# Performance work log

Hardware: AMD Instinct MI355X
Metric: run time of the kernel (lower is better)

Reference implementation:

```python
import jax, jax.numpy as jnp
import numpy as np

H = 512        # hidden_size
E = 512        # embedding_size
VOCAB = 32
OPS = 16
B = 64         # batch of trees
N = 1023       # complete binary tree, depth 9 (2^10 - 1 nodes)
TEMP = 3.0
INT_TYPES_MAX = 1  # types 0 (INT_PO) and 1 (INT_NE) carry a numeric arg


def setup_inputs() -> dict:
    key = jax.random.key(0)
    ks = jax.random.split(key, 12)
    s = 0.05
    return {
        "node_types": jax.random.randint(ks[0], (B, N), 0, VOCAB),
        "node_args": jax.random.normal(ks[1], (B, N), jnp.float32),
        "validity_mask": jax.random.uniform(ks[2], (B, OPS), jnp.float32, 1e-3, 1.0),
        "emb_table": jax.random.normal(ks[3], (VOCAB, E), jnp.float32) * s,
        "W_ih": jax.random.normal(ks[4], (8 * H, E), jnp.float32) * s,
        "W_hh": jax.random.normal(ks[5], (8 * H, 2 * H), jnp.float32) * s,
        "b_ih": jax.random.normal(ks[6], (8 * H,), jnp.float32) * s,
        "b_hh": jax.random.normal(ks[7], (8 * H,), jnp.float32) * s,
        "W1": jax.random.normal(ks[8], (H, H), jnp.float32) * s,
        "b1": jax.random.normal(ks[9], (H,), jnp.float32) * s,
        "W2": jax.random.normal(ks[10], (OPS, H), jnp.float32) * s,
        "b2": jax.random.normal(ks[11], (OPS,), jnp.float32) * s,
    }


def reference(node_types, node_args, validity_mask, emb_table,
              W_ih, W_hh, b_ih, b_hh, W1, b1, W2, b2):
    # --- SympleEmbedding: per-node embedding; int-typed nodes carry arg in last slot
    emb = emb_table[node_types]                                   # [B, N, E]
    is_int = node_types <= INT_TYPES_MAX                          # [B, N]
    emb = emb.at[..., -1].set(jnp.where(is_int, node_args, emb[..., -1]))

    # --- BinaryTreeLSTM, batched level-by-level (heap layout: children of i are 2i+1, 2i+2)
    D = int(np.log2(N + 1)) - 1                                   # depth of internal levels-1 = 9
    h = jnp.zeros((B, N, H), emb.dtype)                           # leaves: zeros
    c = jnp.zeros((B, N, H), emb.dtype)
    bias = b_ih + b_hh
    for d in range(D - 1, -1, -1):                                # bottom-up over internal levels
        idx = np.arange(2 ** d - 1, 2 ** (d + 1) - 1)             # nodes at level d
        left, right = 2 * idx + 1, 2 * idx + 2
        h0 = jnp.concatenate([h[:, left], h[:, right]], axis=-1)  # [B, n, 2H]
        c0 = jnp.concatenate([c[:, left], c[:, right]], axis=-1)
        gates = (jnp.einsum('bne,ge->bng', emb[:, idx], W_ih)
                 + jnp.einsum('bnh,gh->bng', h0, W_hh) + bias)    # [B, n, 8H]
        i_g, f_g, g_g, o_g = jnp.split(gates, 4, axis=-1)         # torch LSTM gate order i,f,g,o
        c_new = jax.nn.sigmoid(f_g) * c0 + jax.nn.sigmoid(i_g) * jnp.tanh(g_g)
        h_new = jax.nn.sigmoid(o_g) * jnp.tanh(c_new)
        h = h.at[:, idx].set(h_new[..., :H])                      # keep first H (as in module)
        c = c.at[:, idx].set(c_new[..., :H])

    # --- actor FFN on root hidden + validity-masked tempered softmax
    root_h = h[:, 0]                                              # [B, H]
    x = jax.nn.relu(root_h @ W1.T + b1)
    logits = x @ W2.T + b2 + jnp.log(validity_mask)
    return jax.nn.softmax(logits / TEMP, axis=-1)                 # [B, OPS]
```

## Files before the change

kernel.cpp:

```cpp
#include <hip/hip_runtime.h>
#include <math.h>

#define Nn 1023

typedef __attribute__((ext_vector_type(8))) short short8;
typedef __attribute__((ext_vector_type(4))) float f32x4;

#define AS1(p) ((const __attribute__((address_space(1))) void*)(p))
#define AS3(p) ((__attribute__((address_space(3))) void*)(p))

__device__ __forceinline__ float sigf(float x) { return 1.0f / (1.0f + __expf(-x)); }
__device__ __forceinline__ float tanhfast(float x) {
    float e = __expf(2.0f * x);
    return 1.0f - 2.0f / (e + 1.0f);
}
__device__ __forceinline__ unsigned short f2bf(float x) {
    unsigned u = __float_as_uint(x);
    return (unsigned short)((u + 0x7fffu + ((u >> 16) & 1u)) >> 16);
}
__device__ __forceinline__ float bf2f(unsigned short b) {
    return __uint_as_float(((unsigned)b) << 16);
}

__global__ __launch_bounds__(256) void pack_whT(const float* __restrict__ W_hh,
                                                unsigned short* __restrict__ WhT) {
    int idx = blockIdx.x * 256 + threadIdx.x;
    int P = idx >> 7;
    int k0 = (idx & 127) * 8;
    int row = ((P >> 4) & 3) * 1024 + (P >> 6) * 16 + (P & 15);
    const float* src = W_hh + (size_t)row * 1024 + k0;
    float4 v0 = *(const float4*)src;
    float4 v1 = *(const float4*)(src + 4);
    short8 o;
    o[0] = (short)f2bf(v0.x); o[1] = (short)f2bf(v0.y);
    o[2] = (short)f2bf(v0.z); o[3] = (short)f2bf(v0.w);
    o[4] = (short)f2bf(v1.x); o[5] = (short)f2bf(v1.y);
    o[6] = (short)f2bf(v1.z); o[7] = (short)f2bf(v1.w);
    *(short8*)(WhT + (size_t)P * 1024 + k0) = o;
}

__global__ __launch_bounds__(256) void transpose512(const float* __restrict__ W1,
                                                    float* __restrict__ W1t) {
    __shared__ float tile[64][65];
    int jb = blockIdx.x * 64, kb = blockIdx.y * 64;
    int t = threadIdx.x;
    #pragma unroll
    for (int i = 0; i < 16; ++i) {
        int idx = t + i * 256;
        int lj = idx >> 6, lk = idx & 63;
        tile[lj][lk] = W1[(jb + lj) * 512 + kb + lk];
    }
    __syncthreads();
    #pragma unroll
    for (int i = 0; i < 16; ++i) {
        int idx = t + i * 256;
        int lk = idx >> 6, lj = idx & 63;
        W1t[(kb + lk) * 512 + jb + lj] = tile[lj][lk];
    }
}

__global__ __launch_bounds__(256) void prep_nodes(
    const int* __restrict__ node_types, const float* __restrict__ node_args,
    const float* __restrict__ emb, const float* __restrict__ W2,
    float* __restrict__ W2t, int* __restrict__ tyv, float* __restrict__ alphaf) {
    int gid = blockIdx.x * 256 + threadIdx.x;
    if (gid < 32704) {
        int node = gid >> 6, b = gid & 63;
        int ty = node_types[b * Nn + node];
        tyv[gid] = ty;
        alphaf[gid] = (ty <= 1) ? (node_args[b * Nn + node] - emb[ty * 512 + 511]) : 0.f;
    }
    if (gid < 8192) {
        int k = gid >> 4, op = gid & 15;
        W2t[gid] = W2[op * 512 + k];
    }
}

__global__ __launch_bounds__(256) void e32_kernel(
    const float* __restrict__ emb, const float* __restrict__ W_ih,
    const float* __restrict__ b_ih, const float* __restrict__ b_hh,
    float* __restrict__ E32b, float* __restrict__ w511f) {
    int o = blockIdx.x * 256 + threadIdx.x;
    int ty = o >> 11, P = o & 2047;
    int row = ((P >> 4) & 3) * 1024 + (P >> 6) * 16 + (P & 15);
    const float* er = emb + (size_t)ty * 512;
    const float* wr = W_ih + (size_t)row * 512;
    float s = b_ih[row] + b_hh[row];
    for (int k = 0; k < 512; k += 4) {
        float4 e4 = *(const float4*)(er + k);
        float4 w4 = *(const float4*)(wr + k);
        s = fmaf(e4.x, w4.x, fmaf(e4.y, w4.y, fmaf(e4.z, w4.z, fmaf(e4.w, w4.w, s))));
    }
    E32b[o] = s;
    if (ty == 0) w511f[P] = wr[511];
}

__global__ __launch_bounds__(256) void leaf_tables(
    const float* __restrict__ E32b,
    unsigned short* __restrict__ Hleaf, float* __restrict__ Hleaf_f,
    float* __restrict__ Cleaf) {
    int o = blockIdx.x * 256 + threadIdx.x;
    int ty = o >> 9, j = o & 511;
    int Pb = (j >> 4) * 64 + (j & 15);
    const float* Er = E32b + (size_t)ty * 2048;
    float ig = Er[Pb], gg = Er[Pb + 32], og = Er[Pb + 48];
    float cn = sigf(ig) * tanhfast(gg);
    float hn = sigf(og) * tanhfast(cn);
    Hleaf[o] = f2bf(hn);
    Hleaf_f[o] = hn;
    Cleaf[o] = cn;
}

__global__ __launch_bounds__(256) void leaf_int(
    const float* __restrict__ E32b, const float* __restrict__ w511f,
    const int* __restrict__ tyv, const float* __restrict__ alphaf,
    unsigned short* __restrict__ Hside, float* __restrict__ Cside) {
    int r = blockIdx.x * 4 + (threadIdx.x >> 6);
    int gn = 16320 + r;
    int ty = tyv[gn];
    if (ty > 1) return;
    float al = alphaf[gn];
    int l = r >> 6, b = r & 63;
    int jc = (threadIdx.x & 63) * 8;
    const float* Er = E32b + (size_t)ty * 2048;
    short8 hv;
    float cv[8];
    #pragma unroll
    for (int jj = 0; jj < 8; ++jj) {
        int j = jc + jj;
        int Pb = (j >> 4) * 64 + (j & 15);
        float ig = Er[Pb]      + al * w511f[Pb];
        float gg = Er[Pb + 32] + al * w511f[Pb + 32];
        float og = Er[Pb + 48] + al * w511f[Pb + 48];
        float cn = sigf(ig) * tanhfast(gg);
        float hn = sigf(og) * tanhfast(cn);
        hv[jj] = (short)f2bf(hn);
        cv[jj] = cn;
    }
    *(short8*)(Hside + (size_t)r * 512 + jc) = hv;
    if ((l & 1) == 0) {
        size_t cr = ((size_t)((l >> 1) * 64 + b)) * 512 + jc;
        float4 c0 = {cv[0], cv[1], cv[2], cv[3]};
        float4 c1 = {cv[4], cv[5], cv[6], cv[7]};
        *(float4*)(Cside + cr) = c0;
        *(float4*)(Cside + cr + 4) = c1;
    }
}

__global__ __launch_bounds__(256) void glgr_kernel(
    const float* __restrict__ W_hh, const float* __restrict__ Hleaf_f,
    float* __restrict__ GLt, float* __restrict__ GRt,
    int* __restrict__ rowidx, int* __restrict__ cnt) {
    int gid = blockIdx.x * 256 + threadIdx.x;
    if (gid < 8448) rowidx[gid] = 0;
    if (gid == 8448) *cnt = 0;
    int side = gid >> 16, ty = (gid >> 11) & 31, P = gid & 2047;
    int row = ((P >> 4) & 3) * 1024 + (P >> 6) * 16 + (P & 15);
    const float* wr = W_hh + (size_t)row * 1024 + side * 512;
    const float* hr = Hleaf_f + (size_t)ty * 512;
    float s = 0.f;
    for (int k = 0; k < 512; k += 4) {
        float4 w4 = *(const float4*)(wr + k);
        float4 h4 = *(const float4*)(hr + k);
        s = fmaf(w4.x, h4.x, fmaf(w4.y, h4.y, fmaf(w4.z, h4.z, fmaf(w4.w, h4.w, s))));
    }
    if (side == 0) GLt[ty * 2048 + P] = s;
    else           GRt[ty * 2048 + P] = s;
}

__global__ __launch_bounds__(256) void flag_k(
    const int* __restrict__ tyv, int* __restrict__ rowidx, int* __restrict__ cnt) {
    int r = blockIdx.x * 256 + threadIdx.x;
    int lf = (r >> 6) * 128 + (r & 63);
    if (tyv[16320 + lf] <= 1 || tyv[16320 + lf + 64] <= 1) {
        int p = atomicAdd(cnt, 1);
        rowidx[p] = r;
    }
}

__global__ void zero_out(float* __restrict__ outp, int n) {
    int i = blockIdx.x * 256 + threadIdx.x;
    if (i < n) outp[i] = 0.f;
}

__global__ __launch_bounds__(256) void d7_table_cell(
    const float* __restrict__ E32b, const float* __restrict__ GLt,
    const float* __restrict__ GRt, const float* __restrict__ Cleaf,
    const float* __restrict__ Cside, const float* __restrict__ w511f,
    const int* __restrict__ tyv, const float* __restrict__ alphaf,
    unsigned short* __restrict__ out_h, float* __restrict__ out_c) {
    __shared__ float Es[32][129];
    __shared__ float GLs[32][129];
    __shared__ float GRs[32][129];
    __shared__ float Cls[32][33];
    __shared__ float w5s[128];
    const int t = threadIdx.x;
    const int j0 = blockIdx.y * 32;
    const int r = blockIdx.x * 256 + t;

    for (int i = t; i < 32 * 128; i += 256) {
        int ty = i >> 7, pp = i & 127;
        int gp = ((j0 >> 4) + (pp >> 6)) * 64 + (pp & 63);
        Es[ty][pp]  = E32b[ty * 2048 + gp];
        GLs[ty][pp] = GLt[ty * 2048 + gp];
        GRs[ty][pp] = GRt[ty * 2048 + gp];
    }
    for (int i = t; i < 32 * 32; i += 256) {
        int ty = i >> 5, jl = i & 31;
        Cls[ty][jl] = Cleaf[ty * 512 + j0 + jl];
    }
    if (t < 128) w5s[t] = w511f[((j0 >> 4) + (t >> 6)) * 64 + (t & 63)];
    __syncthreads();

    int gn = 8128 + r;
    int tyP = tyv[gn];
    float aP = alphaf[gn];
    int lf = (r >> 6) * 128 + (r & 63);
    int tyL = tyv[16320 + lf];
    int tyR = tyv[16320 + lf + 64];
    bool intL = (tyL <= 1);
    bool evenl = (((r >> 6) & 1) == 0);
    size_t crow = ((size_t)((r >> 7) * 64 + (r & 63))) * 512;

    #pragma unroll
    for (int j8 = 0; j8 < 4; ++j8) {
        short8 hv;
        float cv[8];
        #pragma unroll
        for (int jj = 0; jj < 8; ++jj) {
            int jl = j8 * 8 + jj;
            int ppb = (jl >> 4) * 64 + (jl & 15);
            float ig = Es[tyP][ppb]      + aP * w5s[ppb]      + GLs[tyL][ppb]      + GRs[tyR][ppb];
            float fg = Es[tyP][ppb + 16] + aP * w5s[ppb + 16] + GLs[tyL][ppb + 16] + GRs[tyR][ppb + 16];
            float gg = Es[tyP][ppb + 32] + aP * w5s[ppb + 32] + GLs[tyL][ppb + 32] + GRs[tyR][ppb + 32];
            float og = Es[tyP][ppb + 48] + aP * w5s[ppb + 48] + GLs[tyL][ppb + 48] + GRs[tyR][ppb + 48];
            float cl = intL ? Cside[(size_t)r * 512 + j0 + jl] : Cls[tyL][jl];
            float cn = sigf(fg) * cl + sigf(ig) * tanhfast(gg);
            float hn = sigf(og) * tanhfast(cn);
            hv[jj] = (short)f2bf(hn);
            cv[jj] = cn;
        }
        *(short8*)(out_h + (size_t)r * 512 + j0 + j8 * 8) = hv;
        if (evenl) {
            float4 c0 = {cv[0], cv[1], cv[2], cv[3]};
            float4 c1 = {cv[4], cv[5], cv[6], cv[7]};
            *(float4*)(out_c + crow + j0 + j8 * 8) = c0;
            *(float4*)(out_c + crow + j0 + j8 * 8 + 4) = c1;
        }
    }
}

template<int MODE>
__global__ __launch_bounds__(256) void lstm_mfma(
    const unsigned short* __restrict__ WhT, const float* __restrict__ E32b,
    const float* __restrict__ w511f,
    const int* __restrict__ tyv, const float* __restrict__ alphaf,
    const unsigned short* __restrict__ in_h, const float* __restrict__ in_c,
    const unsigned short* __restrict__ Hleaf, const unsigned short* __restrict__ Hside,
    const float* __restrict__ Cleaf, const float* __restrict__ Cside,
    const int* __restrict__ rowidx, const int* __restrict__ cnt,
    unsigned short* __restrict__ out_h, float* __restrict__ out_c,
    int base, int nloc) {
    extern __shared__ unsigned short AB[];
    const int t = threadIdx.x;
    const int w = t >> 6, lane = t & 63;
    const int wr = w >> 1, wc = w & 1;
    const int lane15 = lane & 15, lg = lane >> 4;
    const int M = nloc * 64;
    const int brow0 = blockIdx.x * 128;
    const int bcol0 = blockIdx.y * 128;
    const int lanek8 = (lane & 7) * 8;

    if (MODE == 2) {
        int nc = *cnt;
        int padded = (nc + 127) & ~127;
        if (brow0 >= padded) return;
    }

    const unsigned short* baseL[4];
    const unsigned short* baseR[4];
    const unsigned short* wB[4];
    #pragma unroll
    for (int q = 0; q < 4; ++q) {
        int m = w * 32 + q * 8 + (lane >> 3);
        int r = brow0 + m;
        if (MODE == 2) r = rowidx[r];
        else if (r > M - 1) r = M - 1;
        int lf = (r >> 6) * 128 + (r & 63);
        if (MODE >= 1) {
            int tyL = tyv[16320 + lf];
            int tyR = tyv[16320 + lf + 64];
            baseL[q] = (tyL <= 1) ? (Hside + (size_t)lf * 512)
                                  : (Hleaf + (size_t)tyL * 512);
            baseR[q] = (tyR <= 1) ? (Hside + (size_t)(lf + 64) * 512)
                                  : (Hleaf + (size_t)tyR * 512);
        } else {
            baseL[q] = in_h + (size_t)lf * 512;
            baseR[q] = baseL[q] + 64 * 512;
        }
        int P = bcol0 + w * 32 + q * 8 + (lane >> 3);
        wB[q] = WhT + (size_t)P * 1024;
    }

    auto stage = [&](int kt, int cur) {
        unsigned short* Ad = AB + cur * 16384;
        unsigned short* Bd = Ad + 8192;
        #pragma unroll
        for (int q = 0; q < 4; ++q) {
            const unsigned short* s = (kt < 8) ? (baseL[q] + kt * 64)
                                               : (baseR[q] + (kt - 8) * 64);
            __builtin_amdgcn_global_load_lds(AS1(s + lanek8),
                                             AS3(Ad + w * 2048 + q * 512), 16, 0, 0);
            __builtin_amdgcn_global_load_lds(AS1(wB[q] + kt * 64 + lanek8),
                                             AS3(Bd + w * 2048 + q * 512), 16, 0, 0);
        }
    };

    stage(0, 0);

    f32x4 acc[4][4];
    float w4[4];
    int P4[4];
    int rr[4][4];
    #pragma unroll
    for (int q = 0; q < 4; ++q) {
        P4[q] = bcol0 + wc * 64 + q * 16 + lane15;
        w4[q] = w511f[P4[q]];
    }
    #pragma unroll
    for (int mi = 0; mi < 4; ++mi) {
        #pragma unroll
        for (int reg = 0; reg < 4; ++reg) {
            int r = brow0 + wr * 64 + mi * 16 + lg * 4 + reg;
            if (MODE == 2) r = rowidx[r];
            else if (r > M - 1) r = M - 1;
            rr[mi][reg] = r;
            int gn = base * 64 + r;
            int ty = tyv[gn];
            float al = alphaf[gn];
            const float* Er = E32b + (size_t)ty * 2048;
            #pragma unroll
            for (int q = 0; q < 4; ++q)
                acc[mi][q][reg] = Er[P4[q]] + al * w4[q];
        }
    }

    int cur = 0;
    for (int kt = 0; kt < 16; ++kt) {
        __syncthreads();
        if (kt < 15) stage(kt + 1, cur ^ 1);
        const unsigned short* Ac = AB + cur * 16384;
        const unsigned short* Bc = Ac + 8192;
        #pragma unroll
        for (int ks = 0; ks < 2; ++ks) {
            short8 av[4], bv[4];
            #pragma unroll
            for (int mi = 0; mi < 4; ++mi)
                av[mi] = *(const short8*)(Ac + (wr * 64 + mi * 16 + lane15) * 64 + ks * 32 + lg * 8);
            #pragma unroll
            for (int q = 0; q < 4; ++q)
                bv[q] = *(const short8*)(Bc + (wc * 64 + q * 16 + lane15) * 64 + ks * 32 + lg * 8);
            #pragma unroll
            for (int mi = 0; mi < 4; ++mi)
                #pragma unroll
                for (int q = 0; q < 4; ++q)
                    acc[mi][q] = __builtin_amdgcn_mfma_f32_16x16x32_bf16(av[mi], bv[q], acc[mi][q], 0, 0, 0);
        }
        cur ^= 1;
    }

    const int j = (blockIdx.y * 2 + wc) * 16 + lane15;
    #pragma unroll
    for (int mi = 0; mi < 4; ++mi) {
        #pragma unroll
        for (int reg = 0; reg < 4; ++reg) {
            int r = rr[mi][reg];
            if (r < M) {
                float ig = acc[mi][0][reg];
                float fg = acc[mi][1][reg];
                float gg = acc[mi][2][reg];
                float og = acc[mi][3][reg];
                float cl;
                if (MODE >= 1) {
                    int lf = (r >> 6) * 128 + (r & 63);
                    int tyL = tyv[16320 + lf];
                    cl = (tyL <= 1) ? Cside[(size_t)r * 512 + j]
                                    : Cleaf[(size_t)tyL * 512 + j];
                } else {
                    cl = in_c[(size_t)r * 512 + j];
                }
                float cn = sigf(fg) * cl + sigf(ig) * tanhfast(gg);
                float hn = sigf(og) * tanhfast(cn);
                out_h[(size_t)r * 512 + j] = f2bf(hn);
                if (((r >> 6) & 1) == 0)
                    out_c[((size_t)((r >> 7) * 64 + (r & 63))) * 512 + j] = cn;
            }
        }
    }
}

__global__ __launch_bounds__(256) void head_kernel(
    const unsigned short* __restrict__ rootH, const float* __restrict__ W1t,
    const float* __restrict__ b1, const float* __restrict__ W2t,
    const float* __restrict__ b2, const float* __restrict__ vmask,
    float* __restrict__ outp) {
    __shared__ float rh[512];
    __shared__ float xs[512];
    __shared__ float part[16][17];
    int b = blockIdx.x, t = threadIdx.x;
    rh[t] = bf2f(rootH[b * 512 + t]);
    rh[t + 256] = bf2f(rootH[b * 512 + t + 256]);
    __syncthreads();
    #pragma unroll
    for (int jj = 0; jj < 2; ++jj) {
        int j = t + jj * 256;
        float acc = b1[j];
        for (int k = 0; k < 512; ++k) acc = fmaf(rh[k], W1t[k * 512 + j], acc);
        xs[j] = fmaxf(acc, 0.f);
    }
    __syncthreads();
    int op = t & 15, seg = t >> 4;
    float p = 0.f;
    for (int k = seg * 32; k < seg * 32 + 32; ++k) p = fmaf(xs[k], W2t[k * 16 + op], p);
    part[seg][op] = p;
    __syncthreads();
    if (t < 16) {
        float s = 0.f;
        #pragma unroll
        for (int g = 0; g < 16; ++g) s += part[g][t];
        float logit = s + b2[t] + logf(vmask[b * 16 + t]);
        float z = logit * (1.0f / 3.0f);
        float m = z;
        for (int off = 8; off; off >>= 1) m = fmaxf(m, __shfl_xor(m, off, 16));
        float e = __expf(z - m);
        float ssum = e;
        for (int off = 8; off; off >>= 1) ssum += __shfl_xor(ssum, off, 16);
        outp[b * 16 + t] = e / ssum;
    }
}

extern "C" void kernel_launch(void* const* d_in, const int* in_sizes, int n_in,
                              void* d_out, int out_size, void* d_ws, size_t ws_size,
                              hipStream_t stream) {
    const int*   node_types = (const int*)d_in[0];
    const float* node_args  = (const float*)d_in[1];
    const float* vmask      = (const float*)d_in[2];
    const float* emb_table  = (const float*)d_in[3];
    const float* W_ih       = (const float*)d_in[4];
    const float* W_hh       = (const float*)d_in[5];
    const float* b_ih       = (const float*)d_in[6];
    const float* b_hh       = (const float*)d_in[7];
    const float* W1         = (const float*)d_in[8];
    const float* b1         = (const float*)d_in[9];
    const float* W2         = (const float*)d_in[10];
    const float* b2         = (const float*)d_in[11];
    float* out = (float*)d_out;

    char* ws = (char*)d_ws;
    size_t off = 0;
    auto alloc = [&](size_t bytes) { char* p = ws + off; off += (bytes + 255) & ~(size_t)255; return p; };
    unsigned short* WhT  = (unsigned short*)alloc((size_t)2048 * 1024 * 2);
    float* E32b          = (float*)alloc((size_t)32 * 2048 * 4);
    float* w511f         = (float*)alloc(2048 * 4);
    float* W1t           = (float*)alloc((size_t)512 * 512 * 4);
    float* W2t           = (float*)alloc(8192 * 4);
    int*   tyv           = (int*)alloc(32704 * 4);
    float* alphaf        = (float*)alloc(32704 * 4);
    unsigned short* Hleaf= (unsigned short*)alloc((size_t)32 * 512 * 2);
    float* Hleaf_f       = (float*)alloc((size_t)32 * 512 * 4);
    float* Cleaf         = (float*)alloc((size_t)32 * 512 * 4);
    float* GLt           = (float*)alloc((size_t)32 * 2048 * 4);
    float* GRt           = (float*)alloc((size_t)32 * 2048 * 4);
    int*   rowidx        = (int*)alloc(8448 * 4);
    int*   cnt           = (int*)alloc(256);
    unsigned short* Hside= (unsigned short*)alloc((size_t)16384 * 512 * 2);
    float* Cside         = (float*)alloc((size_t)8192 * 512 * 4);
    unsigned short* Xh   = (unsigned short*)alloc((size_t)8192 * 512 * 2);
    unsigned short* Yh   = (unsigned short*)alloc((size_t)4096 * 512 * 2);
    float* Xc            = (float*)alloc((size_t)4096 * 512 * 4);
    float* Yc            = (float*)alloc((size_t)2048 * 512 * 4);

    if (ws_size < off) {
        zero_out<<<(out_size + 255) / 256, 256, 0, stream>>>(out, out_size);
        return;
    }

    pack_whT<<<1024, 256, 0, stream>>>(W_hh, WhT);
    transpose512<<<dim3(8, 8), 256, 0, stream>>>(W1, W1t);
    prep_nodes<<<128, 256, 0, stream>>>(node_types, node_args, emb_table, W2, W2t, tyv, alphaf);
    e32_kernel<<<256, 256, 0, stream>>>(emb_table, W_ih, b_ih, b_hh, E32b, w511f);
    leaf_tables<<<64, 256, 0, stream>>>(E32b, Hleaf, Hleaf_f, Cleaf);
    leaf_int<<<4096, 256, 0, stream>>>(E32b, w511f, tyv, alphaf, Hside, Cside);
    glgr_kernel<<<512, 256, 0, stream>>>(W_hh, Hleaf_f, GLt, GRt, rowidx, cnt);
    flag_k<<<32, 256, 0, stream>>>(tyv, rowidx, cnt);

    d7_table_cell<<<dim3(32, 16), 256, 0, stream>>>(
        E32b, GLt, GRt, Cleaf, Cside, w511f, tyv, alphaf, Xh, Xc);
    lstm_mfma<2><<<dim3(64, 16), 256, 65536, stream>>>(
        WhT, E32b, w511f, tyv, alphaf,
        nullptr, nullptr, Hleaf, Hside, Cleaf, Cside,
        rowidx, cnt, Xh, Xc, 127, 128);

    for (int d = 6; d >= 0; --d) {
        int nloc = 1 << d;
        unsigned short* oh = (d & 1) ? Xh : Yh;
        float* oc          = (d & 1) ? Xc : Yc;
        const unsigned short* ih = (d & 1) ? Yh : Xh;
        const float* ic          = (d & 1) ? Yc : Xc;
        int gx = (nloc >= 2) ? (nloc / 2) : 1;
        lstm_mfma<0><<<dim3(gx, 16), 256, 65536, stream>>>(
            WhT, E32b, w511f, tyv, alphaf, ih, ic,
            nullptr, nullptr, nullptr, nullptr,
            nullptr, nullptr, oh, oc, nloc - 1, nloc);
    }

    head_kernel<<<64, 256, 0, stream>>>(Yh, W1t, b1, W2t, b2, vmask, out);
}
```

Baseline: 420.0 us.

## Fuse tree LSTM levels into one cooperative persistent kernel with grid syncs

Merges the four prep kernels into one multi-role kernel and folds leaf_int, glgr and flag into another, so there are fewer launches. The d7 table, the MODE-2 level, the upper tree levels and the head now run in one cooperative kernel of 512 blocks, separated by grid-wide syncs. This is meant to remove roughly ten kernel launches and their gaps on a tiny, latency-bound tree recursion. In exchange, the upper levels leave most blocks idle at each grid sync. A fallback keeps the separate launches if occupancy is below two blocks per CU or the cooperative launch fails.

```diff
diff --git a/kernel.cpp b/kernel.cpp
--- a/kernel.cpp
+++ b/kernel.cpp
@@ -1,5 +1,8 @@
 #include <hip/hip_runtime.h>
+#include <hip/hip_cooperative_groups.h>
 #include <math.h>
+
+namespace cg = cooperative_groups;
 
 #define Nn 1023
 
@@ -22,77 +25,78 @@
     return __uint_as_float(((unsigned)b) << 16);
 }
 
-__global__ __launch_bounds__(256) void pack_whT(const float* __restrict__ W_hh,
-                                                unsigned short* __restrict__ WhT) {
-    int idx = blockIdx.x * 256 + threadIdx.x;
-    int P = idx >> 7;
-    int k0 = (idx & 127) * 8;
-    int row = ((P >> 4) & 3) * 1024 + (P >> 6) * 16 + (P & 15);
-    const float* src = W_hh + (size_t)row * 1024 + k0;
-    float4 v0 = *(const float4*)src;
-    float4 v1 = *(const float4*)(src + 4);
-    short8 o;
-    o[0] = (short)f2bf(v0.x); o[1] = (short)f2bf(v0.y);
-    o[2] = (short)f2bf(v0.z); o[3] = (short)f2bf(v0.w);
-    o[4] = (short)f2bf(v1.x); o[5] = (short)f2bf(v1.y);
-    o[6] = (short)f2bf(v1.z); o[7] = (short)f2bf(v1.w);
-    *(short8*)(WhT + (size_t)P * 1024 + k0) = o;
-}
-
-__global__ __launch_bounds__(256) void transpose512(const float* __restrict__ W1,
-                                                    float* __restrict__ W1t) {
-    __shared__ float tile[64][65];
-    int jb = blockIdx.x * 64, kb = blockIdx.y * 64;
-    int t = threadIdx.x;
-    #pragma unroll
-    for (int i = 0; i < 16; ++i) {
-        int idx = t + i * 256;
-        int lj = idx >> 6, lk = idx & 63;
-        tile[lj][lk] = W1[(jb + lj) * 512 + kb + lk];
-    }
-    __syncthreads();
-    #pragma unroll
-    for (int i = 0; i < 16; ++i) {
-        int idx = t + i * 256;
-        int lk = idx >> 6, lj = idx & 63;
-        W1t[(kb + lk) * 512 + jb + lj] = tile[lj][lk];
-    }
-}
-
-__global__ __launch_bounds__(256) void prep_nodes(
+__global__ __launch_bounds__(256) void prep_all(
+    const float* __restrict__ W_hh, unsigned short* __restrict__ WhT,
+    const float* __restrict__ W1, float* __restrict__ W1t,
     const int* __restrict__ node_types, const float* __restrict__ node_args,
     const float* __restrict__ emb, const float* __restrict__ W2,
-    float* __restrict__ W2t, int* __restrict__ tyv, float* __restrict__ alphaf) {
-    int gid = blockIdx.x * 256 + threadIdx.x;
-    if (gid < 32704) {
-        int node = gid >> 6, b = gid & 63;
-        int ty = node_types[b * Nn + node];
-        tyv[gid] = ty;
-        alphaf[gid] = (ty <= 1) ? (node_args[b * Nn + node] - emb[ty * 512 + 511]) : 0.f;
-    }
-    if (gid < 8192) {
-        int k = gid >> 4, op = gid & 15;
-        W2t[gid] = W2[op * 512 + k];
-    }
-}
-
-__global__ __launch_bounds__(256) void e32_kernel(
-    const float* __restrict__ emb, const float* __restrict__ W_ih,
-    const float* __restrict__ b_ih, const float* __restrict__ b_hh,
-    float* __restrict__ E32b, float* __restrict__ w511f) {
-    int o = blockIdx.x * 256 + threadIdx.x;
-    int ty = o >> 11, P = o & 2047;
-    int row = ((P >> 4) & 3) * 1024 + (P >> 6) * 16 + (P & 15);
-    const float* er = emb + (size_t)ty * 512;
-    const float* wr = W_ih + (size_t)row * 512;
-    float s = b_ih[row] + b_hh[row];
-    for (int k = 0; k < 512; k += 4) {
-        float4 e4 = *(const float4*)(er + k);
-        float4 w4 = *(const float4*)(wr + k);
-        s = fmaf(e4.x, w4.x, fmaf(e4.y, w4.y, fmaf(e4.z, w4.z, fmaf(e4.w, w4.w, s))));
-    }
-    E32b[o] = s;
-    if (ty == 0) w511f[P] = wr[511];
+    float* __restrict__ W2t, int* __restrict__ tyv, float* __restrict__ alphaf,
+    const float* __restrict__ W_ih, const float* __restrict__ b_ih,
+    const float* __restrict__ b_hh, float* __restrict__ E32b,
+    float* __restrict__ w511f, int* __restrict__ rowidx, int* __restrict__ cnt) {
+    int bid = blockIdx.x, t = threadIdx.x;
+    if (bid < 1024) {
+        int idx = bid * 256 + t;
+        int P = idx >> 7;
+        int k0 = (idx & 127) * 8;
+        int row = ((P >> 4) & 3) * 1024 + (P >> 6) * 16 + (P & 15);
+        const float* src = W_hh + (size_t)row * 1024 + k0;
+        float4 v0 = *(const float4*)src;
+        float4 v1 = *(const float4*)(src + 4);
+        short8 o;
+        o[0] = (short)f2bf(v0.x); o[1] = (short)f2bf(v0.y);
+        o[2] = (short)f2bf(v0.z); o[3] = (short)f2bf(v0.w);
+        o[4] = (short)f2bf(v1.x); o[5] = (short)f2bf(v1.y);
+        o[6] = (short)f2bf(v1.z); o[7] = (short)f2bf(v1.w);
+        *(short8*)(WhT + (size_t)P * 1024 + k0) = o;
+    } else if (bid < 1088) {
+        __shared__ float tile[64][65];
+        int idx2 = bid - 1024;
+        int jb = (idx2 & 7) * 64, kb = (idx2 >> 3) * 64;
+        #pragma unroll
+        for (int i = 0; i < 16; ++i) {
+            int idx = t + i * 256;
+            int lj = idx >> 6, lk = idx & 63;
+            tile[lj][lk] = W1[(jb + lj) * 512 + kb + lk];
+        }
+        __syncthreads();
+        #pragma unroll
+        for (int i = 0; i < 16; ++i) {
+            int idx = t + i * 256;
+            int lk = idx >> 6, lj = idx & 63;
+            W1t[(kb + lk) * 512 + jb + lj] = tile[lj][lk];
+        }
+    } else if (bid < 1216) {
+        int gid = (bid - 1088) * 256 + t;
+        if (gid < 32704) {
+            int node = gid >> 6, b = gid & 63;
+            int ty = node_types[b * Nn + node];
+            tyv[gid] = ty;
+            alphaf[gid] = (ty <= 1) ? (node_args[b * Nn + node] - emb[ty * 512 + 511]) : 0.f;
+        }
+        if (gid < 8192) {
+            int k = gid >> 4, op = gid & 15;
+            W2t[gid] = W2[op * 512 + k];
+        }
+    } else if (bid < 1472) {
+        int o = (bid - 1216) * 256 + t;
+        int ty = o >> 11, P = o & 2047;
+        int row = ((P >> 4) & 3) * 1024 + (P >> 6) * 16 + (P & 15);
+        const float* er = emb + (size_t)ty * 512;
+        const float* wr = W_ih + (size_t)row * 512;
+        float s = b_ih[row] + b_hh[row];
+        for (int k = 0; k < 512; k += 4) {
+            float4 e4 = *(const float4*)(er + k);
+            float4 w4 = *(const float4*)(wr + k);
+            s = fmaf(e4.x, w4.x, fmaf(e4.y, w4.y, fmaf(e4.z, w4.z, fmaf(e4.w, w4.w, s))));
+        }
+        E32b[o] = s;
+        if (ty == 0) w511f[P] = wr[511];
+    } else {
+        int z = (bid - 1472) * 256 + t;
+        if (z < 8448) rowidx[z] = 0;
+        if (bid == 1472 && t == 0) *cnt = 0;
+    }
 }
 
 __global__ __launch_bounds__(256) void leaf_tables(
@@ -111,70 +115,66 @@
     Cleaf[o] = cn;
 }
 
-__global__ __launch_bounds__(256) void leaf_int(
+__global__ __launch_bounds__(256) void leaf_side(
     const float* __restrict__ E32b, const float* __restrict__ w511f,
     const int* __restrict__ tyv, const float* __restrict__ alphaf,
-    unsigned short* __restrict__ Hside, float* __restrict__ Cside) {
-    int r = blockIdx.x * 4 + (threadIdx.x >> 6);
-    int gn = 16320 + r;
-    int ty = tyv[gn];
-    if (ty > 1) return;
-    float al = alphaf[gn];
-    int l = r >> 6, b = r & 63;
-    int jc = (threadIdx.x & 63) * 8;
-    const float* Er = E32b + (size_t)ty * 2048;
-    short8 hv;
-    float cv[8];
-    #pragma unroll
-    for (int jj = 0; jj < 8; ++jj) {
-        int j = jc + jj;
-        int Pb = (j >> 4) * 64 + (j & 15);
-        float ig = Er[Pb]      + al * w511f[Pb];
-        float gg = Er[Pb + 32] + al * w511f[Pb + 32];
-        float og = Er[Pb + 48] + al * w511f[Pb + 48];
-        float cn = sigf(ig) * tanhfast(gg);
-        float hn = sigf(og) * tanhfast(cn);
-        hv[jj] = (short)f2bf(hn);
-        cv[jj] = cn;
-    }
-    *(short8*)(Hside + (size_t)r * 512 + jc) = hv;
-    if ((l & 1) == 0) {
-        size_t cr = ((size_t)((l >> 1) * 64 + b)) * 512 + jc;
-        float4 c0 = {cv[0], cv[1], cv[2], cv[3]};
-        float4 c1 = {cv[4], cv[5], cv[6], cv[7]};
-        *(float4*)(Cside + cr) = c0;
-        *(float4*)(Cside + cr + 4) = c1;
-    }
-}
-
-__global__ __launch_bounds__(256) void glgr_kernel(
+    unsigned short* __restrict__ Hside, float* __restrict__ Cside,
     const float* __restrict__ W_hh, const float* __restrict__ Hleaf_f,
     float* __restrict__ GLt, float* __restrict__ GRt,
     int* __restrict__ rowidx, int* __restrict__ cnt) {
-    int gid = blockIdx.x * 256 + threadIdx.x;
-    if (gid < 8448) rowidx[gid] = 0;
-    if (gid == 8448) *cnt = 0;
-    int side = gid >> 16, ty = (gid >> 11) & 31, P = gid & 2047;
-    int row = ((P >> 4) & 3) * 1024 + (P >> 6) * 16 + (P & 15);
-    const float* wr = W_hh + (size_t)row * 1024 + side * 512;
-    const float* hr = Hleaf_f + (size_t)ty * 512;
-    float s = 0.f;
-    for (int k = 0; k < 512; k += 4) {
-        float4 w4 = *(const float4*)(wr + k);
-        float4 h4 = *(const float4*)(hr + k);
-        s = fmaf(w4.x, h4.x, fmaf(w4.y, h4.y, fmaf(w4.z, h4.z, fmaf(w4.w, h4.w, s))));
-    }
-    if (side == 0) GLt[ty * 2048 + P] = s;
-    else           GRt[ty * 2048 + P] = s;
-}
-
-__global__ __launch_bounds__(256) void flag_k(
-    const int* __restrict__ tyv, int* __restrict__ rowidx, int* __restrict__ cnt) {
-    int r = blockIdx.x * 256 + threadIdx.x;
-    int lf = (r >> 6) * 128 + (r & 63);
-    if (tyv[16320 + lf] <= 1 || tyv[16320 + lf + 64] <= 1) {
-        int p = atomicAdd(cnt, 1);
-        rowidx[p] = r;
+    int bid = blockIdx.x, t = threadIdx.x;
+    if (bid < 4096) {
+        int r = bid * 4 + (t >> 6);
+        int gn = 16320 + r;
+        int ty = tyv[gn];
+        if (ty > 1) return;
+        float al = alphaf[gn];
+        int l = r >> 6, b = r & 63;
+        int jc = (t & 63) * 8;
+        const float* Er = E32b + (size_t)ty * 2048;
+        short8 hv;
+        float cv[8];
+        #pragma unroll
+        for (int jj = 0; jj < 8; ++jj) {
+            int j = jc + jj;
+            int Pb = (j >> 4) * 64 + (j & 15);
+            float ig = Er[Pb]      + al * w511f[Pb];
+            float gg = Er[Pb + 32] + al * w511f[Pb + 32];
+            float og = Er[Pb + 48] + al * w511f[Pb + 48];
+            float cn = sigf(ig) * tanhfast(gg);
+            float hn = sigf(og) * tanhfast(cn);
+            hv[jj] = (short)f2bf(hn);
+            cv[jj] = cn;
+        }
+        *(short8*)(Hside + (size_t)r * 512 + jc) = hv;
+        if ((l & 1) == 0) {
+            size_t cr = ((size_t)((l >> 1) * 64 + b)) * 512 + jc;
+            float4 c0 = {cv[0], cv[1], cv[2], cv[3]};
+            float4 c1 = {cv[4], cv[5], cv[6], cv[7]};
+            *(float4*)(Cside + cr) = c0;
+            *(float4*)(Cside + cr + 4) = c1;
+        }
+    } else if (bid < 4608) {
+        int gid = (bid - 4096) * 256 + t;
+        int side = gid >> 16, ty = (gid >> 11) & 31, P = gid & 2047;
+        int row = ((P >> 4) & 3) * 1024 + (P >> 6) * 16 + (P & 15);
+        const float* wr = W_hh + (size_t)row * 1024 + side * 512;
+        const float* hr = Hleaf_f + (size_t)ty * 512;
+        float s = 0.f;
+        for (int k = 0; k < 512; k += 4) {
+            float4 w4 = *(const float4*)(wr + k);
+            float4 h4 = *(const float4*)(hr + k);
+            s = fmaf(w4.x, h4.x, fmaf(w4.y, h4.y, fmaf(w4.z, h4.z, fmaf(w4.w, h4.w, s))));
+        }
+        if (side == 0) GLt[ty * 2048 + P] = s;
+        else           GRt[ty * 2048 + P] = s;
+    } else {
+        int r = (bid - 4608) * 256 + t;
+        int lf = (r >> 6) * 128 + (r & 63);
+        if (tyv[16320 + lf] <= 1 || tyv[16320 + lf + 64] <= 1) {
+            int p = atomicAdd(cnt, 1);
+            rowidx[p] = r;
+        }
     }
 }
 
@@ -183,31 +183,33 @@
     if (i < n) outp[i] = 0.f;
 }
 
-__global__ __launch_bounds__(256) void d7_table_cell(
+__device__ __forceinline__ void d7_table_body(
+    char* smemraw,
     const float* __restrict__ E32b, const float* __restrict__ GLt,
     const float* __restrict__ GRt, const float* __restrict__ Cleaf,
     const float* __restrict__ Cside, const float* __restrict__ w511f,
     const int* __restrict__ tyv, const float* __restrict__ alphaf,
-    unsigned short* __restrict__ out_h, float* __restrict__ out_c) {
-    __shared__ float Es[32][129];
-    __shared__ float GLs[32][129];
-    __shared__ float GRs[32][129];
-    __shared__ float Cls[32][33];
-    __shared__ float w5s[128];
+    unsigned short* __restrict__ out_h, float* __restrict__ out_c,
+    int bx, int by) {
+    float* Es  = (float*)smemraw;
+    float* GLs = Es + 32 * 129;
+    float* GRs = GLs + 32 * 129;
+    float* Cls = GRs + 32 * 129;
+    float* w5s = Cls + 32 * 33;
     const int t = threadIdx.x;
-    const int j0 = blockIdx.y * 32;
-    const int r = blockIdx.x * 256 + t;
+    const int j0 = by * 32;
+    const int r = bx * 256 + t;
 
     for (int i = t; i < 32 * 128; i += 256) {
         int ty = i >> 7, pp = i & 127;
         int gp = ((j0 >> 4) + (pp >> 6)) * 64 + (pp & 63);
-        Es[ty][pp]  = E32b[ty * 2048 + gp];
-        GLs[ty][pp] = GLt[ty * 2048 + gp];
-        GRs[ty][pp] = GRt[ty * 2048 + gp];
+        Es[ty * 129 + pp]  = E32b[ty * 2048 + gp];
+        GLs[ty * 129 + pp] = GLt[ty * 2048 + gp];
+        GRs[ty * 129 + pp] = GRt[ty * 2048 + gp];
     }
     for (int i = t; i < 32 * 32; i += 256) {
         int ty = i >> 5, jl = i & 31;
-        Cls[ty][jl] = Cleaf[ty * 512 + j0 + jl];
+        Cls[ty * 33 + jl] = Cleaf[ty * 512 + j0 + jl];
     }
     if (t < 128) w5s[t] = w511f[((j0 >> 4) + (t >> 6)) * 64 + (t & 63)];
     __syncthreads();
@@ -230,11 +232,11 @@
         for (int jj = 0; jj < 8; ++jj) {
             int jl = j8 * 8 + jj;
             int ppb = (jl >> 4) * 64 + (jl & 15);
-            float ig = Es[tyP][ppb]      + aP * w5s[ppb]      + GLs[tyL][ppb]      + GRs[tyR][ppb];
-            float fg = Es[tyP][ppb + 16] + aP * w5s[ppb + 16] + GLs[tyL][ppb + 16] + GRs[tyR][ppb + 16];
-            float gg = Es[tyP][ppb + 32] + aP * w5s[ppb + 32] + GLs[tyL][ppb + 32] + GRs[tyR][ppb + 32];
-            float og = Es[tyP][ppb + 48] + aP * w5s[ppb + 48] + GLs[tyL][ppb + 48] + GRs[tyR][ppb + 48];
-            float cl = intL ? Cside[(size_t)r * 512 + j0 + jl] : Cls[tyL][jl];
+            float ig = Es[tyP * 129 + ppb]      + aP * w5s[ppb]      + GLs[tyL * 129 + ppb]      + GRs[tyR * 129 + ppb];
+            float fg = Es[tyP * 129 + ppb + 16] + aP * w5s[ppb + 16] + GLs[tyL * 129 + ppb + 16] + GRs[tyR * 129 + ppb + 16];
+            float gg = Es[tyP * 129 + ppb + 32] + aP * w5s[ppb + 32] + GLs[tyL * 129 + ppb + 32] + GRs[tyR * 129 + ppb + 32];
+            float og = Es[tyP * 129 + ppb + 48] + aP * w5s[ppb + 48] + GLs[tyL * 129 + ppb + 48] + GRs[tyR * 129 + ppb + 48];
+            float cl = intL ? Cside[(size_t)r * 512 + j0 + jl] : Cls[tyL * 33 + jl];
             float cn = sigf(fg) * cl + sigf(ig) * tanhfast(gg);
             float hn = sigf(og) * tanhfast(cn);
             hv[jj] = (short)f2bf(hn);
@@ -248,34 +250,30 @@
             *(float4*)(out_c + crow + j0 + j8 * 8 + 4) = c1;
         }
     }
+    __syncthreads();
 }
 
 template<int MODE>
-__global__ __launch_bounds__(256) void lstm_mfma(
+__device__ __forceinline__ void mfma_tile(
+    char* smemraw,
     const unsigned short* __restrict__ WhT, const float* __restrict__ E32b,
     const float* __restrict__ w511f,
     const int* __restrict__ tyv, const float* __restrict__ alphaf,
     const unsigned short* __restrict__ in_h, const float* __restrict__ in_c,
     const unsigned short* __restrict__ Hleaf, const unsigned short* __restrict__ Hside,
     const float* __restrict__ Cleaf, const float* __restrict__ Cside,
-    const int* __restrict__ rowidx, const int* __restrict__ cnt,
+    const int* __restrict__ rowidx,
     unsigned short* __restrict__ out_h, float* __restrict__ out_c,
-    int base, int nloc) {
-    extern __shared__ unsigned short AB[];
+    int base, int nloc, int bx, int by) {
+    unsigned short* AB = (unsigned short*)smemraw;
     const int t = threadIdx.x;
     const int w = t >> 6, lane = t & 63;
     const int wr = w >> 1, wc = w & 1;
     const int lane15 = lane & 15, lg = lane >> 4;
     const int M = nloc * 64;
-    const int brow0 = blockIdx.x * 128;
-    const int bcol0 = blockIdx.y * 128;
+    const int brow0 = bx * 128;
+    const int bcol0 = by * 128;
     const int lanek8 = (lane & 7) * 8;
-
-    if (MODE == 2) {
-        int nc = *cnt;
-        int padded = (nc + 127) & ~127;
-        if (brow0 >= padded) return;
-    }
 
     const unsigned short* baseL[4];
     const unsigned short* baseR[4];
@@ -369,7 +367,7 @@
         cur ^= 1;
     }
 
-    const int j = (blockIdx.y * 2 + wc) * 16 + lane15;
+    const int j = (by * 2 + wc) * 16 + lane15;
     #pragma unroll
     for (int mi = 0; mi < 4; ++mi) {
         #pragma unroll
@@ -399,44 +397,135 @@
     }
 }
 
-__global__ __launch_bounds__(256) void head_kernel(
+__device__ __forceinline__ void head_body(
+    char* smemraw,
     const unsigned short* __restrict__ rootH, const float* __restrict__ W1t,
     const float* __restrict__ b1, const float* __restrict__ W2t,
     const float* __restrict__ b2, const float* __restrict__ vmask,
-    float* __restrict__ outp) {
-    __shared__ float rh[512];
-    __shared__ float xs[512];
-    __shared__ float part[16][17];
-    int b = blockIdx.x, t = threadIdx.x;
+    float* __restrict__ outp, int b) {
+    float* rh = (float*)smemraw;
+    float* xs = rh + 512;
+    float* part = xs + 512;
+    int t = threadIdx.x;
     rh[t] = bf2f(rootH[b * 512 + t]);
     rh[t + 256] = bf2f(rootH[b * 512 + t + 256]);
     __syncthreads();
     #pragma unroll
     for (int jj = 0; jj < 2; ++jj) {
-        int j = t + jj * 256;
-        float acc = b1[j];
-        for (int k = 0; k < 512; ++k) acc = fmaf(rh[k], W1t[k * 512 + j], acc);
-        xs[j] = fmaxf(acc, 0.f);
+        int jx = t + jj * 256;
+        float acc = b1[jx];
+        for (int k = 0; k < 512; ++k) acc = fmaf(rh[k], W1t[k * 512 + jx], acc);
+        xs[jx] = fmaxf(acc, 0.f);
     }
     __syncthreads();
     int op = t & 15, seg = t >> 4;
     float p = 0.f;
     for (int k = seg * 32; k < seg * 32 + 32; ++k) p = fmaf(xs[k], W2t[k * 16 + op], p);
-    part[seg][op] = p;
+    part[seg * 17 + op] = p;
     __syncthreads();
     if (t < 16) {
         float s = 0.f;
         #pragma unroll
-        for (int g = 0; g < 16; ++g) s += part[g][t];
+        for (int g = 0; g < 16; ++g) s += part[g * 17 + t];
         float logit = s + b2[t] + logf(vmask[b * 16 + t]);
         float z = logit * (1.0f / 3.0f);
         float m = z;
-        for (int off = 8; off; off >>= 1) m = fmaxf(m, __shfl_xor(m, off, 16));
+        for (int o2 = 8; o2; o2 >>= 1) m = fmaxf(m, __shfl_xor(m, o2, 16));
         float e = __expf(z - m);
         float ssum = e;
-        for (int off = 8; off; off >>= 1) ssum += __shfl_xor(ssum, off, 16);
+        for (int o2 = 8; o2; o2 >>= 1) ssum += __shfl_xor(ssum, o2, 16);
         outp[b * 16 + t] = e / ssum;
     }
+}
+
+__global__ __launch_bounds__(256) void tree_main(
+    const unsigned short* WhT, const float* E32b, const float* w511f,
+    const int* tyv, const float* alphaf,
+    const unsigned short* Hleaf, const unsigned short* Hside,
+    const float* Cleaf, const float* Cside,
+    const float* GLt, const float* GRt,
+    const int* rowidx, const int* cnt,
+    unsigned short* Xh, float* Xc, unsigned short* Yh, float* Yc,
+    const float* W1t, const float* b1, const float* W2t, const float* b2,
+    const float* vmask, float* outp) {
+    cg::grid_group grid = cg::this_grid();
+    extern __shared__ char smem[];
+    const int bid = blockIdx.x;
+
+    d7_table_body(smem, E32b, GLt, GRt, Cleaf, Cside, w511f, tyv, alphaf,
+                  Xh, Xc, bid & 31, bid >> 5);
+    __threadfence(); grid.sync();
+
+    {
+        int nc = *cnt;
+        int rb = ((nc + 127) & ~127) >> 7;
+        int ntiles = rb * 16;
+        for (int T = bid; T < ntiles; T += 512)
+            mfma_tile<2>(smem, WhT, E32b, w511f, tyv, alphaf, nullptr, nullptr,
+                         Hleaf, Hside, Cleaf, Cside, rowidx,
+                         Xh, Xc, 127, 128, T % rb, T / rb);
+    }
+    __threadfence(); grid.sync();
+
+    for (int d = 6; d >= 0; --d) {
+        int nloc = 1 << d;
+        int gx = (nloc >= 2) ? (nloc >> 1) : 1;
+        unsigned short* oh = (d & 1) ? Xh : Yh;
+        float* oc          = (d & 1) ? Xc : Yc;
+        const unsigned short* ih = (d & 1) ? Yh : Xh;
+        const float* ic          = (d & 1) ? Yc : Xc;
+        int ntiles = gx * 16;
+        if (bid < ntiles)
+            mfma_tile<0>(smem, WhT, E32b, w511f, tyv, alphaf, ih, ic,
+                         nullptr, nullptr, nullptr, nullptr, nullptr,
+                         oh, oc, nloc - 1, nloc, bid % gx, bid / gx);
+        __threadfence(); grid.sync();
+    }
+
+    if (bid < 64)
+        head_body(smem, Yh, W1t, b1, W2t, b2, vmask, outp, bid);
+}
+
+__global__ __launch_bounds__(256) void d7_table_cell_k(
+    const float* __restrict__ E32b, const float* __restrict__ GLt,
+    const float* __restrict__ GRt, const float* __restrict__ Cleaf,
+    const float* __restrict__ Cside, const float* __restrict__ w511f,
+    const int* __restrict__ tyv, const float* __restrict__ alphaf,
+    unsigned short* __restrict__ out_h, float* __restrict__ out_c) {
+    extern __shared__ char smem[];
+    d7_table_body(smem, E32b, GLt, GRt, Cleaf, Cside, w511f, tyv, alphaf,
+                  out_h, out_c, blockIdx.x, blockIdx.y);
+}
+
+template<int MODE>
+__global__ __launch_bounds__(256) void lstm_mfma_k(
+    const unsigned short* __restrict__ WhT, const float* __restrict__ E32b,
+    const float* __restrict__ w511f,
+    const int* __restrict__ tyv, const float* __restrict__ alphaf,
+    const unsigned short* __restrict__ in_h, const float* __restrict__ in_c,
+    const unsigned short* __restrict__ Hleaf, const unsigned short* __restrict__ Hside,
+    const float* __restrict__ Cleaf, const float* __restrict__ Cside,
+    const int* __restrict__ rowidx, const int* __restrict__ cnt,
+    unsigned short* __restrict__ out_h, float* __restrict__ out_c,
+    int base, int nloc) {
+    extern __shared__ char smem[];
+    if (MODE == 2) {
+        int nc = *cnt;
+        int padded = (nc + 127) & ~127;
+        if ((int)blockIdx.x * 128 >= padded) return;
+    }
+    mfma_tile<MODE>(smem, WhT, E32b, w511f, tyv, alphaf, in_h, in_c,
+                    Hleaf, Hside, Cleaf, Cside, rowidx,
+                    out_h, out_c, base, nloc, blockIdx.x, blockIdx.y);
+}
+
+__global__ __launch_bounds__(256) void head_k(
+    const unsigned short* __restrict__ rootH, const float* __restrict__ W1t,
+    const float* __restrict__ b1, const float* __restrict__ W2t,
+    const float* __restrict__ b2, const float* __restrict__ vmask,
+    float* __restrict__ outp) {
+    extern __shared__ char smem[];
+    head_body(smem, rootH, W1t, b1, W2t, b2, vmask, outp, blockIdx.x);
 }
 
 extern "C" void kernel_launch(void* const* d_in, const int* in_sizes, int n_in,
@@ -485,34 +574,58 @@
         return;
     }
 
-    pack_whT<<<1024, 256, 0, stream>>>(W_hh, WhT);
-    transpose512<<<dim3(8, 8), 256, 0, stream>>>(W1, W1t);
-    prep_nodes<<<128, 256, 0, stream>>>(node_types, node_args, emb_table, W2, W2t, tyv, alphaf);
-    e32_kernel<<<256, 256, 0, stream>>>(emb_table, W_ih, b_ih, b_hh, E32b, w511f);
+    prep_all<<<1505, 256, 0, stream>>>(W_hh, WhT, W1, W1t, node_types, node_args,
+                                       emb_table, W2, W2t, tyv, alphaf,
+                                       W_ih, b_ih, b_hh, E32b, w511f, rowidx, cnt);
     leaf_tables<<<64, 256, 0, stream>>>(E32b, Hleaf, Hleaf_f, Cleaf);
-    leaf_int<<<4096, 256, 0, stream>>>(E32b, w511f, tyv, alphaf, Hside, Cside);
-    glgr_kernel<<<512, 256, 0, stream>>>(W_hh, Hleaf_f, GLt, GRt, rowidx, cnt);
-    flag_k<<<32, 256, 0, stream>>>(tyv, rowidx, cnt);
-
-    d7_table_cell<<<dim3(32, 16), 256, 0, stream>>>(
-        E32b, GLt, GRt, Cleaf, Cside, w511f, tyv, alphaf, Xh, Xc);
-    lstm_mfma<2><<<dim3(64, 16), 256, 65536, stream>>>(
-        WhT, E32b, w511f, tyv, alphaf,
-        nullptr, nullptr, Hleaf, Hside, Cleaf, Cside,
-        rowidx, cnt, Xh, Xc, 127, 128);
-
-    for (int d = 6; d >= 0; --d) {
-        int nloc = 1 << d;
-        unsigned short* oh = (d & 1) ? Xh : Yh;
-        float* oc          = (d & 1) ? Xc : Yc;
-        const unsigned short* ih = (d & 1) ? Yh : Xh;
-        const float* ic          = (d & 1) ? Yc : Xc;
-        int gx = (nloc >= 2) ? (nloc / 2) : 1;
-        lstm_mfma<0><<<dim3(gx, 16), 256, 65536, stream>>>(
-            WhT, E32b, w511f, tyv, alphaf, ih, ic,
-            nullptr, nullptr, nullptr, nullptr,
-            nullptr, nullptr, oh, oc, nloc - 1, nloc);
-    }
-
-    head_kernel<<<64, 256, 0, stream>>>(Yh, W1t, b1, W2t, b2, vmask, out);
-}
+    leaf_side<<<4640, 256, 0, stream>>>(E32b, w511f, tyv, alphaf, Hside, Cside,
+                                        W_hh, Hleaf_f, GLt, GRt, rowidx, cnt);
+
+    bool coop_ok = false;
+    {
+        int occ = 0;
+        hipError_t qe = hipOccupancyMaxActiveBlocksPerMultiprocessor(
+            &occ, tree_main, 256, 65536);
+        if (qe == hipSuccess && occ >= 2) coop_ok = true;
+    }
+    if (coop_ok) {
+        const unsigned short* cWhT = WhT;  const float* cE32b = E32b;
+        const float* cw511 = w511f;        const int* ctyv = tyv;
+        const float* calpha = alphaf;      const unsigned short* cHleaf = Hleaf;
+        const unsigned short* cHside = Hside; const float* cCleaf = Cleaf;
+        const float* cCside = Cside;       const float* cGL = GLt;
+        const float* cGR = GRt;            const int* cridx = rowidx;
+        const int* ccnt = cnt;             const float* cW1t = W1t;
+        const float* cW2t = W2t;
+        void* kargs[] = {
+            (void*)&cWhT, (void*)&cE32b, (void*)&cw511, (void*)&ctyv, (void*)&calpha,
+            (void*)&cHleaf, (void*)&cHside, (void*)&cCleaf, (void*)&cCside,
+            (void*)&cGL, (void*)&cGR, (void*)&cridx, (void*)&ccnt,
+            (void*)&Xh, (void*)&Xc, (void*)&Yh, (void*)&Yc,
+            (void*)&cW1t, (void*)&b1, (void*)&cW2t, (void*)&b2,
+            (void*)&vmask, (void*)&out };
+        hipError_t le = hipLaunchCooperativeKernel(
+            tree_main, dim3(512), dim3(256), kargs, (unsigned)65536, stream);
+        if (le != hipSuccess) coop_ok = false;
+    }
+    if (!coop_ok) {
+        d7_table_cell_k<<<dim3(32, 16), 256, 54272, stream>>>(
+            E32b, GLt, GRt, Cleaf, Cside, w511f, tyv, alphaf, Xh, Xc);
+        lstm_mfma_k<2><<<dim3(64, 16), 256, 65536, stream>>>(
+            WhT, E32b, w511f, tyv, alphaf, nullptr, nullptr,
+            Hleaf, Hside, Cleaf, Cside, rowidx, cnt, Xh, Xc, 127, 128);
+        for (int d = 6; d >= 0; --d) {
+            int nloc = 1 << d;
+            unsigned short* oh = (d & 1) ? Xh : Yh;
+            float* oc          = (d & 1) ? Xc : Yc;
+            const unsigned short* ih = (d & 1) ? Yh : Xh;
+            const float* ic          = (d & 1) ? Yc : Xc;
+            int gx = (nloc >= 2) ? (nloc / 2) : 1;
+            lstm_mfma_k<0><<<dim3(gx, 16), 256, 65536, stream>>>(
+                WhT, E32b, w511f, tyv, alphaf, ih, ic,
+                nullptr, nullptr, nullptr, nullptr,
+                nullptr, nullptr, oh, oc, nloc - 1, nloc);
+        }
+        head_k<<<64, 256, 5184, stream>>>(Yh, W1t, b1, W2t, b2, vmask, out);
+    }
+}
```

After: 448.8 us. 1.07x slower.
